# Kernel tuning notes

Measured on AMD Instinct MI355X. Metric: run time of the kernel, lower is better.

Reference implementation:

```python
import jax, jax.numpy as jnp
import numpy as np

ALPHA = 0.2        # LeakyReLU negative slope used in standard GAT
NEG_INF = -9e15    # mask fill value from the canonical pyGAT implementation


def _gat_layer(x, adj_mask, W, a1, a2, concat):
    """One GAT attention head.
    x: [B,N,Din], adj_mask: [B,N,N] bool, W: [Din,Dout], a1/a2: [Dout].
    """
    Wh = jnp.einsum('bnd,df->bnf', x, W)               # [B,N,Dout]
    f1 = jnp.einsum('bnf,f->bn', Wh, a1)               # source scores
    f2 = jnp.einsum('bnf,f->bn', Wh, a2)               # target scores
    e = jax.nn.leaky_relu(f1[:, :, None] + f2[:, None, :], ALPHA)  # [B,N,N]
    e = jnp.where(adj_mask, e, jnp.float32(NEG_INF))
    attn = jax.nn.softmax(e, axis=-1)                  # masked row-softmax
    out = jnp.einsum('bnm,bmf->bnf', attn, Wh)         # neighbor aggregation
    return jax.nn.elu(out) if concat else out


def setup_inputs() -> dict:
    key = jax.random.key(0)
    ks = jax.random.split(key, 8)
    B, N, Din, Dout, H = 32, 512, 768, 256, 8
    x = jax.random.normal(ks[0], (B, N, Din), jnp.float32)
    adj = jax.random.randint(ks[1], (B, N, N), 0, 2, jnp.int32)  # {0,1} adjacency
    W0 = jax.random.normal(ks[2], (H, Din, Dout), jnp.float32) * (1.0 / np.sqrt(Din))
    a1_0 = jax.random.normal(ks[3], (H, Dout), jnp.float32) * 0.1
    a2_0 = jax.random.normal(ks[4], (H, Dout), jnp.float32) * 0.1
    Wo = jax.random.normal(ks[5], (Dout, Dout), jnp.float32) * (1.0 / np.sqrt(Dout))
    a1_o = jax.random.normal(ks[6], (Dout,), jnp.float32) * 0.1
    a2_o = jax.random.normal(ks[7], (Dout,), jnp.float32) * 0.1
    return dict(x=x, adj=adj, W0=W0, a1_0=a1_0, a2_0=a2_0,
                Wo=Wo, a1_o=a1_o, a2_o=a2_o)


def reference(x, adj, W0, a1_0, a2_0, Wo, a1_o, a2_o):
    mask = adj > 0
    # multi-head layer: vmap over heads replaces the Python head loop
    heads = jax.vmap(lambda W, a1, a2: _gat_layer(x, mask, W, a1, a2, True))(
        W0, a1_0, a2_0)                                # [H,B,N,Dout]
    h = heads.mean(axis=0)                             # cat+unsqueeze+mean(dim=1)
    # dropout is identity in eval mode (p effectively 0 for the baseline)
    out = _gat_layer(h, mask, Wo, a1_o, a2_o, False)   # gat_out, concat=False
    return jax.nn.relu(out)                            # [B,N,Dout]
```

## Files before the change

kernel.cpp:

```cpp
#include <hip/hip_runtime.h>
#include <hip/hip_bf16.h>
#include <stdint.h>

typedef __bf16 bf16;
typedef short short8 __attribute__((ext_vector_type(8)));
typedef float f32x4 __attribute__((ext_vector_type(4)));

#define LOG2E 1.4426950408889634f

union V16 { uint4 u; short8 s; bf16 h[8]; };
union U8  { ushort4 s; bf16 h[4]; };

typedef const __attribute__((address_space(1))) void* gp_t;
typedef __attribute__((address_space(3))) void* lp_t;
__device__ __forceinline__ void gld16(const bf16* g, bf16* l) {
  __builtin_amdgcn_global_load_lds((gp_t)g, (lp_t)l, 16, 0, 0);
}

__global__ __launch_bounds__(256) void k_prep(float4* __restrict__ zp, int zn4,
                                              const float* __restrict__ cs,
                                              bf16* __restrict__ cd,
                                              const int* __restrict__ adj,
                                              unsigned long long* __restrict__ mask,
                                              const float* __restrict__ W0,
                                              bf16* __restrict__ W0T,
                                              const float* __restrict__ Wo,
                                              bf16* __restrict__ WoT) {
  __shared__ float t[32][33];
  int id = blockIdx.x;
  const int tid = threadIdx.x;
  if (id < 288) {
    int i = id * 256 + tid;
    if (i < zn4) zp[i] = {0.f, 0.f, 0.f, 0.f};
    return;
  }
  id -= 288;
  if (id < 6144) {
    long long i = ((long long)id * 256 + tid) * 8;
    float4 a = *(const float4*)(cs + i);
    float4 b = *(const float4*)(cs + i + 4);
    U8 w0, w1;
    w0.h[0] = (bf16)a.x; w0.h[1] = (bf16)a.y; w0.h[2] = (bf16)a.z; w0.h[3] = (bf16)a.w;
    w1.h[0] = (bf16)b.x; w1.h[1] = (bf16)b.y; w1.h[2] = (bf16)b.z; w1.h[3] = (bf16)b.w;
    *(ushort4*)(cd + i)     = w0.s;
    *(ushort4*)(cd + i + 4) = w1.s;
    return;
  }
  id -= 6144;
  if (id < 32768) {
    int wid = id * 4 + (tid >> 6);
    int lane = tid & 63;
    int a = adj[(long long)wid * 64 + lane];
    unsigned long long m = __ballot(a > 0);
    if (lane == 0) mask[wid] = m;
    return;
  }
  id -= 32768;
  const float* src; bf16* dst; int R, C, bx, by, bz;
  if (id < 1536) {
    src = W0; dst = W0T; R = 768; C = 256;
    bx = id & 7; by = (id >> 3) % 24; bz = id / 192;
  } else {
    id -= 1536;
    src = Wo; dst = WoT; R = 256; C = 256;
    bx = id & 7; by = id >> 3; bz = 0;
  }
  src += (long long)bz * R * C;
  dst += (long long)bz * R * C;
  int c0 = bx * 32, r0 = by * 32;
  int tx = tid & 31, ty = tid >> 5;
  for (int rr = ty; rr < 32; rr += 8)
    t[rr][tx] = src[(long long)(r0 + rr) * C + (c0 + tx)];
  __syncthreads();
  for (int cc = ty; cc < 32; cc += 8)
    dst[(long long)(c0 + cc) * R + (r0 + tx)] = (bf16)t[tx][cc];
}

__global__ __launch_bounds__(256) void k_gemm(const bf16* __restrict__ A,
                                              const bf16* __restrict__ WT,
                                              bf16* __restrict__ outT, int K,
                                              const float* __restrict__ a1,
                                              const float* __restrict__ a2,
                                              int aStride,
                                              float* __restrict__ f1out,
                                              float* __restrict__ f2out) {
  __shared__ bf16 As[128 * 32];
  __shared__ bf16 Bs[128 * 32];
  const int nb = blockIdx.x, mb = blockIdx.y, h = blockIdx.z;
  const int tid = threadIdx.x, wave = tid >> 6, lane = tid & 63;
  const int lrow = lane & 15, quad = lane >> 4;
  const long long mbase = (long long)mb * 128;
  const int nbase = nb * 128;
  const bf16* W = WT + (long long)h * 256 * K;
  const int wm = (wave >> 1) * 64, wn = (wave & 1) * 64;
  const int srow = wave * 16 + (lane >> 2);
  const int skoff = (lane & 3) * 8;
  const bf16* ag0 = A + (mbase + srow) * K + skoff;
  const bf16* ag1 = ag0 + 64 * K;
  const bf16* bg0 = W + (long long)(nbase + srow) * K + skoff;
  const bf16* bg1 = bg0 + 64 * K;
  bf16* lA0 = As + wave * 16 * 32;
  bf16* lA1 = As + (64 + wave * 16) * 32;
  bf16* lB0 = Bs + wave * 16 * 32;
  bf16* lB1 = Bs + (64 + wave * 16) * 32;
  f32x4 acc[4][4];
#pragma unroll
  for (int i = 0; i < 4; i++)
#pragma unroll
    for (int j = 0; j < 4; j++) acc[i][j] = {0.f, 0.f, 0.f, 0.f};
  for (int k0 = 0; k0 < K; k0 += 32) {
    __syncthreads();
    gld16(ag0 + k0, lA0);
    gld16(ag1 + k0, lA1);
    gld16(bg0 + k0, lB0);
    gld16(bg1 + k0, lB1);
    __syncthreads();
    V16 af[4], bfx[4];
#pragma unroll
    for (int mi = 0; mi < 4; mi++)
      af[mi].u = *(const uint4*)(As + (wm + mi * 16 + lrow) * 32 + quad * 8);
#pragma unroll
    for (int ni = 0; ni < 4; ni++)
      bfx[ni].u = *(const uint4*)(Bs + (wn + ni * 16 + lrow) * 32 + quad * 8);
#pragma unroll
    for (int mi = 0; mi < 4; mi++)
#pragma unroll
      for (int ni = 0; ni < 4; ni++)
        acc[mi][ni] = __builtin_amdgcn_mfma_f32_16x16x32_bf16(af[mi].s, bfx[ni].s, acc[mi][ni], 0, 0, 0);
  }
#pragma unroll
  for (int mi = 0; mi < 4; mi++) {
    long long m0 = mbase + wm + mi * 16 + quad * 4;
    int bbi = (int)(m0 >> 9);
    int jj = (int)(m0 & 511);
    int js = jj >> 5, qp = (jj >> 3) & 3, eo = jj & 7;
    long long rowbase = (long long)(h * 32 + bbi) * 131072 +
                        (long long)js * 512 + (qp * 16 + lrow) * 8 + eo;
#pragma unroll
    for (int ni = 0; ni < 4; ni++) {
      int ft = ((nbase + wn) >> 4) + ni;
      U8 w;
#pragma unroll
      for (int r = 0; r < 4; r++) w.h[r] = (bf16)acc[mi][ni][r];
      *(ushort4*)(outT + rowbase + (long long)ft * 8192) = w.s;
    }
  }
  float av1[4], av2[4];
#pragma unroll
  for (int ni = 0; ni < 4; ni++) {
    int f = nbase + wn + ni * 16 + lrow;
    av1[ni] = a1[h * aStride + f];
    av2[ni] = a2[h * aStride + f];
  }
#pragma unroll
  for (int mi = 0; mi < 4; mi++) {
#pragma unroll
    for (int r = 0; r < 4; r++) {
      float s1 = 0.f, s2 = 0.f;
#pragma unroll
      for (int ni = 0; ni < 4; ni++) {
        s1 = __builtin_fmaf(acc[mi][ni][r], av1[ni], s1);
        s2 = __builtin_fmaf(acc[mi][ni][r], av2[ni], s2);
      }
#pragma unroll
      for (int off = 1; off < 16; off <<= 1) {
        s1 += __shfl_xor(s1, off);
        s2 += __shfl_xor(s2, off);
      }
      if (lrow == 0) {
        long long m0 = mbase + wm + mi * 16 + quad * 4 + r;
        atomicAdd(&f1out[(long long)h * 16384 + m0], s1);
        atomicAdd(&f2out[(long long)h * 16384 + m0], s2);
      }
    }
  }
}

__global__ __launch_bounds__(256) void k_passA(const float* __restrict__ f1p,
                                               const float* __restrict__ f2p,
                                               const unsigned long long* __restrict__ mask,
                                               float* __restrict__ cc) {
  const int hb = blockIdx.x, bb = hb & 31;
  const int wave = threadIdx.x >> 6, lane = threadIdx.x & 63;
  const int i = blockIdx.y * 4 + wave;
  const float* f2 = f2p + hb * 512;
  float4 va = *(const float4*)(f2 + lane * 8);
  float4 vb = *(const float4*)(f2 + lane * 8 + 4);
  float vj[8] = {va.x, va.y, va.z, va.w, vb.x, vb.y, vb.z, vb.w};
  unsigned int mb = ((const unsigned char*)(mask + ((long long)bb * 512 + i) * 8))[lane];
  float f1 = f1p[hb * 512 + i];
  float m = -INFINITY;
#pragma unroll
  for (int t = 0; t < 8; t++)
    if ((mb >> t) & 1) m = fmaxf(m, vj[t]);
#pragma unroll
  for (int off = 32; off; off >>= 1) m = fmaxf(m, __shfl_xor(m, off));
  float s = f1 + m;
  float M2 = LOG2E * fmaxf(s, 0.2f * s);
  float d = 0.f;
#pragma unroll
  for (int t = 0; t < 8; t++) {
    float e0 = f1 + vj[t];
    float e = fmaxf(e0, 0.2f * e0);
    float p = exp2f(__builtin_fmaf(LOG2E, e, -M2));
    d += ((mb >> t) & 1) ? p : 0.f;
  }
#pragma unroll
  for (int off = 32; off; off >>= 1) d += __shfl_xor(d, off);
  if (lane == 0) {
    float cv = M2 + log2f(d);
    if (!isfinite(M2) || !(d > 0.f)) cv = INFINITY;
    cc[hb * 512 + i] = cv;
  }
}

__device__ __forceinline__ int pchunk(int row, int c) {
  return row * 512 + (((c + 3 * row) & 63) << 3);
}

template <int NSPLIT, int NHB, int ROWS, int MODE>
__global__ __launch_bounds__(256) void k_pv(const bf16* __restrict__ WhT,
                                            const float* __restrict__ f1p,
                                            const float* __restrict__ cc,
                                            const float* __restrict__ f2p,
                                            const unsigned long long* __restrict__ mask,
                                            void* __restrict__ out0,
                                            void* __restrict__ out1) {
  constexpr int TPR = 256 / ROWS;
  constexpr int NT  = 64 / TPR;
  constexpr int MI  = ROWS / 16;
  constexpr int RB  = 32 * (512 / ROWS);
  constexpr int CPT = 256 / TPR;
  __shared__ union { bf16 P[2][ROWS * 512]; float hs[ROWS * 264]; } sh;
  __shared__ unsigned char ms[ROWS * 64];
  const int id = blockIdx.x;
  const int hp = id / RB;
  const int rid = id % RB;
  const int bb = rid & 31, it = rid >> 5;
  const int ibase = it * ROWS;
  const int tid = threadIdx.x, wave = tid >> 6, lane = tid & 63;
  const int lrow = lane & 15, quad = lane >> 4;
  const int pi = tid / TPR;
  const int pj = tid % TPR;
  {
    const uint4* msrc = (const uint4*)(mask + ((long long)bb * 512 + ibase) * 8);
    if (tid < ROWS * 4) ((uint4*)ms)[tid] = msrc[tid];
  }
  __syncthreads();
  unsigned long long mreg = 0;
#pragma unroll
  for (int t = 0; t < NT; t++)
    mreg |= (unsigned long long)ms[pi * 64 + pj + t * TPR] << (t * 8);
  f32x4 hacc[MI][4];
#pragma unroll
  for (int i = 0; i < MI; i++)
#pragma unroll
    for (int j = 0; j < 4; j++) hacc[i][j] = {0.f, 0.f, 0.f, 0.f};

  auto buildP = [&](int h, int buf) {
    const int hb = h * 32 + bb;
    const float f1v = f1p[hb * 512 + ibase + pi];
    const float cv  = cc[hb * 512 + ibase + pi];
    const float Ac = __builtin_fmaf(LOG2E, f1v, -cv);
    const float Bc = __builtin_fmaf(0.2f * LOG2E, f1v, -cv);
    const float* f2 = f2p + hb * 512;
#pragma unroll
    for (int t = 0; t < NT; t++) {
      const int ch = pj + t * TPR;
      const int j0 = ch * 8;
      float4 u0 = *(const float4*)(f2 + j0);
      float4 u1 = *(const float4*)(f2 + j0 + 4);
      float fj[8] = {u0.x, u0.y, u0.z, u0.w, u1.x, u1.y, u1.z, u1.w};
      unsigned int mb = (unsigned int)(mreg >> (t * 8)) & 0xff;
      V16 pk;
#pragma unroll
      for (int u = 0; u < 8; u++) {
        float e = fmaxf(__builtin_fmaf(LOG2E, fj[u], Ac),
                        __builtin_fmaf(0.2f * LOG2E, fj[u], Bc));
        float p = ((mb >> u) & 1) ? exp2f(e) : 0.f;
        pk.h[u] = (bf16)p;
      }
      *(uint4*)(sh.P[buf] + pchunk(pi, ch)) = pk.u;
    }
  };

  buildP(hp * NHB, 0);
  __syncthreads();
#pragma unroll 1
  for (int hh = 0; hh < NHB; hh++) {
    const int h = hp * NHB + hh;
    const int hb = h * 32 + bb;
    if (hh + 1 < NHB) buildP(h + 1, (hh + 1) & 1);
    const bf16* Pb = sh.P[hh & 1];
    const bf16* wfb = WhT + (long long)hb * 131072 + (long long)wave * 32768 + lane * 8;
    f32x4 acc[MI][4];
#pragma unroll
    for (int i = 0; i < MI; i++)
#pragma unroll
      for (int j = 0; j < 4; j++) acc[i][j] = {0.f, 0.f, 0.f, 0.f};
#pragma unroll
    for (int js = 0; js < 16; js++) {
      V16 af[MI], bfr[4];
#pragma unroll
      for (int mi = 0; mi < MI; mi++)
        af[mi].u = *(const uint4*)(Pb + pchunk(mi * 16 + lrow, js * 4 + quad));
#pragma unroll
      for (int ni = 0; ni < 4; ni++)
        bfr[ni].u = *(const uint4*)(wfb + ni * 8192 + js * 512);
#pragma unroll
      for (int ni = 0; ni < 4; ni++)
#pragma unroll
        for (int mi = 0; mi < MI; mi++)
          acc[mi][ni] = __builtin_amdgcn_mfma_f32_16x16x32_bf16(af[mi].s, bfr[ni].s, acc[mi][ni], 0, 0, 0);
    }
    __syncthreads();
#pragma unroll
    for (int mi = 0; mi < MI; mi++)
#pragma unroll
      for (int ni = 0; ni < 4; ni++)
#pragma unroll
        for (int r = 0; r < 4; r++) {
          float v = acc[mi][ni][r];
          hacc[mi][ni][r] += (MODE == 1) ? v
                           : (v > 0.f ? v : (exp2f(v * LOG2E) - 1.f));
        }
  }
#pragma unroll
  for (int mi = 0; mi < MI; mi++)
#pragma unroll
    for (int ni = 0; ni < 4; ni++) {
      int f = wave * 64 + ni * 16 + lrow;
#pragma unroll
      for (int r = 0; r < 4; r++) {
        int row = mi * 16 + quad * 4 + r;
        sh.hs[row * 264 + f] = hacc[mi][ni][r];
      }
    }
  __syncthreads();
  const int fb = pj * CPT;
  float* op = (float*)(hp ? out1 : out0) +
              (((long long)bb * 512) + ibase + pi) * 256 + fb;
#pragma unroll
  for (int c0 = 0; c0 < CPT; c0 += 4) {
    float4 w;
    w.x = sh.hs[pi * 264 + fb + c0 + 0];
    w.y = sh.hs[pi * 264 + fb + c0 + 1];
    w.z = sh.hs[pi * 264 + fb + c0 + 2];
    w.w = sh.hs[pi * 264 + fb + c0 + 3];
    if (MODE == 1) {
      w.x = fmaxf(w.x, 0.f); w.y = fmaxf(w.y, 0.f);
      w.z = fmaxf(w.z, 0.f); w.w = fmaxf(w.w, 0.f);
    }
    *(float4*)(op + c0) = w;
  }
}

__global__ __launch_bounds__(256) void k_fin(const float* __restrict__ a,
                                             const float* __restrict__ b,
                                             bf16* __restrict__ dst) {
  long long i = ((long long)blockIdx.x * 256 + threadIdx.x) * 4;
  float4 x = *(const float4*)(a + i);
  float4 y = *(const float4*)(b + i);
  U8 w;
  w.h[0] = (bf16)((x.x + y.x) * 0.125f);
  w.h[1] = (bf16)((x.y + y.y) * 0.125f);
  w.h[2] = (bf16)((x.z + y.z) * 0.125f);
  w.h[3] = (bf16)((x.w + y.w) * 0.125f);
  *(ushort4*)(dst + i) = w.s;
}

extern "C" void kernel_launch(void* const* d_in, const int* in_sizes, int n_in,
                              void* d_out, int out_size, void* d_ws, size_t ws_size,
                              hipStream_t stream) {
  const float* x    = (const float*)d_in[0];
  const int*   adj  = (const int*)d_in[1];
  const float* W0   = (const float*)d_in[2];
  const float* a1_0 = (const float*)d_in[3];
  const float* a2_0 = (const float*)d_in[4];
  const float* Wo   = (const float*)d_in[5];
  const float* a1_o = (const float*)d_in[6];
  const float* a2_o = (const float*)d_in[7];

  char* p = (char*)d_ws;
  auto take = [&](size_t n) { char* r = p; p += (n + 255) & ~(size_t)255; return r; };
  unsigned long long* maskb = (unsigned long long*)take(32ull * 512 * 8 * 8);
  bf16*  xb   = (bf16*)take(32ull * 512 * 768 * 2);
  bf16*  W0T  = (bf16*)take(8ull * 256 * 768 * 2);
  bf16*  WoT  = (bf16*)take(256ull * 256 * 2);
  bf16*  WhT  = (bf16*)take(8ull * 32 * 256 * 512 * 2);
  float* f1p1 = (float*)take(8ull * 32 * 512 * 4);
  float* f2p1 = (float*)take(8ull * 32 * 512 * 4);
  float* f1p2 = (float*)take(32ull * 512 * 4);
  float* f2p2 = (float*)take(32ull * 512 * 4);
  float* c1   = (float*)take(8ull * 32 * 512 * 4);
  float* c2   = (float*)take(32ull * 512 * 4);
  float* pv1  = (float*)take(32ull * 512 * 256 * 4);
  float* pv0  = (float*)xb;
  bf16*  hmid = (bf16*)((char*)xb + 16ull * 1024 * 1024);
  bf16*  Wh2T = WhT;

  k_prep<<<40800, 256, 0, stream>>>((float4*)f1p1, 73728,
                                    x, xb, adj, maskb,
                                    W0, W0T, Wo, WoT);
  k_gemm<<<dim3(2, 128, 8), 256, 0, stream>>>(xb, W0T, WhT, 768,
                                              a1_0, a2_0, 256, f1p1, f2p1);
  k_passA<<<dim3(256, 128), 256, 0, stream>>>(f1p1, f2p1, maskb, c1);
  k_pv<2, 4, 16, 0><<<2048, 256, 0, stream>>>(WhT, f1p1, c1, f2p1, maskb, pv0, pv1);
  k_fin<<<4096, 256, 0, stream>>>(pv0, pv1, hmid);
  k_gemm<<<dim3(2, 128, 1), 256, 0, stream>>>(hmid, WoT, Wh2T, 256,
                                              a1_o, a2_o, 0, f1p2, f2p2);
  k_passA<<<dim3(32, 128), 256, 0, stream>>>(f1p2, f2p2, maskb, c2);
  k_pv<1, 1, 16, 1><<<1024, 256, 0, stream>>>(Wh2T, f1p2, c2, f2p2, maskb, d_out, nullptr);
}
```

Before: 394.0 us.

## Fuse softmax statistics pass into PV kernel with deferred normalization

Removes the separate k_passA kernel that computed per-row log-sum-exp constants, and instead computes the row max and denominator inside buildP of k_pv via intra-row shuffles. The unnormalized probabilities are written to shared memory and the PV accumulator is scaled by 1/d, stored in a small shared array, before ELU accumulation. This saves two launches and the extra read of f1/f2/mask plus the c buffer writes. In exchange each block does an extra pass over f2 to find the max and more shuffles, and the P values are now unnormalized before bf16 conversion.

```diff
diff --git a/kernel.cpp b/kernel.cpp
--- a/kernel.cpp
+++ b/kernel.cpp
@@ -176,44 +176,6 @@
   }
 }
 
-__global__ __launch_bounds__(256) void k_passA(const float* __restrict__ f1p,
-                                               const float* __restrict__ f2p,
-                                               const unsigned long long* __restrict__ mask,
-                                               float* __restrict__ cc) {
-  const int hb = blockIdx.x, bb = hb & 31;
-  const int wave = threadIdx.x >> 6, lane = threadIdx.x & 63;
-  const int i = blockIdx.y * 4 + wave;
-  const float* f2 = f2p + hb * 512;
-  float4 va = *(const float4*)(f2 + lane * 8);
-  float4 vb = *(const float4*)(f2 + lane * 8 + 4);
-  float vj[8] = {va.x, va.y, va.z, va.w, vb.x, vb.y, vb.z, vb.w};
-  unsigned int mb = ((const unsigned char*)(mask + ((long long)bb * 512 + i) * 8))[lane];
-  float f1 = f1p[hb * 512 + i];
-  float m = -INFINITY;
-#pragma unroll
-  for (int t = 0; t < 8; t++)
-    if ((mb >> t) & 1) m = fmaxf(m, vj[t]);
-#pragma unroll
-  for (int off = 32; off; off >>= 1) m = fmaxf(m, __shfl_xor(m, off));
-  float s = f1 + m;
-  float M2 = LOG2E * fmaxf(s, 0.2f * s);
-  float d = 0.f;
-#pragma unroll
-  for (int t = 0; t < 8; t++) {
-    float e0 = f1 + vj[t];
-    float e = fmaxf(e0, 0.2f * e0);
-    float p = exp2f(__builtin_fmaf(LOG2E, e, -M2));
-    d += ((mb >> t) & 1) ? p : 0.f;
-  }
-#pragma unroll
-  for (int off = 32; off; off >>= 1) d += __shfl_xor(d, off);
-  if (lane == 0) {
-    float cv = M2 + log2f(d);
-    if (!isfinite(M2) || !(d > 0.f)) cv = INFINITY;
-    cc[hb * 512 + i] = cv;
-  }
-}
-
 __device__ __forceinline__ int pchunk(int row, int c) {
   return row * 512 + (((c + 3 * row) & 63) << 3);
 }
@@ -221,7 +183,6 @@
 template <int NSPLIT, int NHB, int ROWS, int MODE>
 __global__ __launch_bounds__(256) void k_pv(const bf16* __restrict__ WhT,
                                             const float* __restrict__ f1p,
-                                            const float* __restrict__ cc,
                                             const float* __restrict__ f2p,
                                             const unsigned long long* __restrict__ mask,
                                             void* __restrict__ out0,
@@ -232,6 +193,7 @@
   constexpr int RB  = 32 * (512 / ROWS);
   constexpr int CPT = 256 / TPR;
   __shared__ union { bf16 P[2][ROWS * 512]; float hs[ROWS * 264]; } sh;
+  __shared__ float dinv[2][ROWS];
   __shared__ unsigned char ms[ROWS * 64];
   const int id = blockIdx.x;
   const int hp = id / RB;
@@ -259,11 +221,26 @@
 
   auto buildP = [&](int h, int buf) {
     const int hb = h * 32 + bb;
-    const float f1v = f1p[hb * 512 + ibase + pi];
-    const float cv  = cc[hb * 512 + ibase + pi];
-    const float Ac = __builtin_fmaf(LOG2E, f1v, -cv);
-    const float Bc = __builtin_fmaf(0.2f * LOG2E, f1v, -cv);
-    const float* f2 = f2p + hb * 512;
+    const float F1L = LOG2E * f1p[hb * 512 + ibase + pi];
+    const float* f2 = f2p + (long long)hb * 512;
+    float mx = -INFINITY;
+#pragma unroll
+    for (int t = 0; t < NT; t++) {
+      const int j0 = (pj + t * TPR) * 8;
+      float4 u0 = *(const float4*)(f2 + j0);
+      float4 u1 = *(const float4*)(f2 + j0 + 4);
+      float fj[8] = {u0.x, u0.y, u0.z, u0.w, u1.x, u1.y, u1.z, u1.w};
+      unsigned int mb = (unsigned int)(mreg >> (t * 8)) & 0xff;
+#pragma unroll
+      for (int u = 0; u < 8; u++) {
+        float a = __builtin_fmaf(LOG2E, fj[u], F1L);
+        float e = fmaxf(a, 0.2f * a);
+        mx = fmaxf(mx, ((mb >> u) & 1) ? e : -INFINITY);
+      }
+    }
+#pragma unroll
+    for (int off = 1; off < TPR; off <<= 1) mx = fmaxf(mx, __shfl_xor(mx, off));
+    float d = 0.f;
 #pragma unroll
     for (int t = 0; t < NT; t++) {
       const int ch = pj + t * TPR;
@@ -275,13 +252,17 @@
       V16 pk;
 #pragma unroll
       for (int u = 0; u < 8; u++) {
-        float e = fmaxf(__builtin_fmaf(LOG2E, fj[u], Ac),
-                        __builtin_fmaf(0.2f * LOG2E, fj[u], Bc));
-        float p = ((mb >> u) & 1) ? exp2f(e) : 0.f;
+        float a = __builtin_fmaf(LOG2E, fj[u], F1L);
+        float e = fmaxf(a, 0.2f * a);
+        float p = ((mb >> u) & 1) ? exp2f(e - mx) : 0.f;
         pk.h[u] = (bf16)p;
+        d += p;
       }
       *(uint4*)(sh.P[buf] + pchunk(pi, ch)) = pk.u;
     }
+#pragma unroll
+    for (int off = 1; off < TPR; off <<= 1) d += __shfl_xor(d, off);
+    if (pj == 0) dinv[buf][pi] = (d > 0.f) ? (1.f / d) : 0.f;
   };
 
   buildP(hp * NHB, 0);
@@ -313,17 +294,23 @@
         for (int mi = 0; mi < MI; mi++)
           acc[mi][ni] = __builtin_amdgcn_mfma_f32_16x16x32_bf16(af[mi].s, bfr[ni].s, acc[mi][ni], 0, 0, 0);
     }
-    __syncthreads();
+    float di[MI][4];
 #pragma unroll
     for (int mi = 0; mi < MI; mi++)
 #pragma unroll
+      for (int r = 0; r < 4; r++)
+        di[mi][r] = dinv[hh & 1][mi * 16 + quad * 4 + r];
+#pragma unroll
+    for (int mi = 0; mi < MI; mi++)
+#pragma unroll
       for (int ni = 0; ni < 4; ni++)
 #pragma unroll
         for (int r = 0; r < 4; r++) {
-          float v = acc[mi][ni][r];
+          float v = acc[mi][ni][r] * di[mi][r];
           hacc[mi][ni][r] += (MODE == 1) ? v
                            : (v > 0.f ? v : (exp2f(v * LOG2E) - 1.f));
         }
+    __syncthreads();
   }
 #pragma unroll
   for (int mi = 0; mi < MI; mi++)
@@ -392,8 +379,6 @@
   float* f2p1 = (float*)take(8ull * 32 * 512 * 4);
   float* f1p2 = (float*)take(32ull * 512 * 4);
   float* f2p2 = (float*)take(32ull * 512 * 4);
-  float* c1   = (float*)take(8ull * 32 * 512 * 4);
-  float* c2   = (float*)take(32ull * 512 * 4);
   float* pv1  = (float*)take(32ull * 512 * 256 * 4);
   float* pv0  = (float*)xb;
   bf16*  hmid = (bf16*)((char*)xb + 16ull * 1024 * 1024);
@@ -404,11 +389,9 @@
                                     W0, W0T, Wo, WoT);
   k_gemm<<<dim3(2, 128, 8), 256, 0, stream>>>(xb, W0T, WhT, 768,
                                               a1_0, a2_0, 256, f1p1, f2p1);
-  k_passA<<<dim3(256, 128), 256, 0, stream>>>(f1p1, f2p1, maskb, c1);
-  k_pv<2, 4, 16, 0><<<2048, 256, 0, stream>>>(WhT, f1p1, c1, f2p1, maskb, pv0, pv1);
+  k_pv<2, 4, 16, 0><<<2048, 256, 0, stream>>>(WhT, f1p1, f2p1, maskb, pv0, pv1);
   k_fin<<<4096, 256, 0, stream>>>(pv0, pv1, hmid);
   k_gemm<<<dim3(2, 128, 1), 256, 0, stream>>>(hmid, WoT, Wh2T, 256,
                                               a1_o, a2_o, 0, f1p2, f2p2);
-  k_passA<<<dim3(32, 128), 256, 0, stream>>>(f1p2, f2p2, maskb, c2);
-  k_pv<1, 1, 16, 1><<<1024, 256, 0, stream>>>(Wh2T, f1p2, c2, f2p2, maskb, d_out, nullptr);
-}
+  k_pv<1, 1, 16, 1><<<1024, 256, 0, stream>>>(Wh2T, f1p2, f2p2, maskb, d_out, nullptr);
+}
```

Result: no change. 386.9 us (-1.8%).
